# Kernel optimization log

Measured on AMD Instinct MI355X. Metric: run time of the kernel, lower is better.

The kernel has to match this reference:

```python
import jax, jax.numpy as jnp
import numpy as np

EPS = 1e-08  # smooth in CELoss


def _lovasz_grad(fg_sorted):
    # Alg. 1 of the Lovasz-Softmax paper; fg_sorted: [P] floats in {0,1}
    gts = fg_sorted.sum()
    intersection = gts - jnp.cumsum(fg_sorted)
    union = gts + jnp.cumsum(1.0 - fg_sorted)
    jaccard = 1.0 - intersection / union
    # first-difference: jaccard[1:] - jaccard[:-1], keep jaccard[0]
    return jnp.concatenate([jaccard[:1], jaccard[1:] - jaccard[:-1]])


def setup_inputs() -> dict:
    key = jax.random.key(0)
    k1, k2 = jax.random.split(key)
    B, C, D, H, W = 1, 3, 96, 256, 256
    probas = jax.random.normal(k1, (B, C, D, H, W), dtype=jnp.float32)
    cls = jax.random.randint(k2, (B, D, H, W), 0, C)
    # one-hot label volume [B, C, D, H, W], matching labels[0][c] == 1 usage
    labels = jax.nn.one_hot(cls, C, axis=1, dtype=jnp.int32)
    weight = jnp.ones((C,), dtype=jnp.float32)  # weight=[1,1,1]
    return {"probas": probas, "weight": weight, "labels": labels}


def reference(probas, weight, labels):
    C = probas.shape[1]
    # flatten_probas (dim==5 path): softmax over classes, flatten to [P, C]
    p = jax.nn.softmax(probas, axis=1)
    p = jnp.moveaxis(p, 1, -1).reshape(-1, C)
    # label reconstruction: 0*ch0 + 1*ch1 + 2*ch2 from one-hot channels
    lab = (labels[0, 1] + 2 * labels[0, 2]).reshape(-1)  # [P] int class ids

    total = jnp.zeros((), dtype=p.dtype)
    count = jnp.zeros((), dtype=p.dtype)
    for c in range(C):
        fg = (lab == c).astype(p.dtype)              # [P]
        present = fg.sum() > 0                       # classes='present'
        # CELoss(softmax=False, average='None'): -fg * log(pred + eps)
        errors = -fg * jnp.log(p[:, c] + EPS)        # [P]
        order = jnp.argsort(-errors)                 # descending sort perm
        errors_sorted = errors[order]
        fg_sorted = fg[order]
        g = jax.lax.stop_gradient(_lovasz_grad(fg_sorted))
        loss_c = weight[c] * jnp.dot(errors_sorted, g)
        total = total + jnp.where(present, loss_c, 0.0)
        count = count + jnp.where(present, 1.0, 0.0)
    # mean over present classes (empty -> 0)
    return jnp.where(count > 0, total / jnp.maximum(count, 1.0), 0.0)
```

## Files before the change

kernel.cpp:

```cpp
#include <hip/hip_runtime.h>


#define EPS 1e-8f
#define BLK 256
#define GPT 6
#define GPB (GPT*BLK)

typedef float fx4 __attribute__((ext_vector_type(4)));
typedef int   ix4 __attribute__((ext_vector_type(4)));

__device__ __forceinline__ void px_acc(float za, float zb, float zc, int la, int lb,
                                       float& s0, float& s1, float& s2,
                                       float& n0, float& n1, float& n2)
{
    float ea = __expf(za);
    float eb = __expf(zb);
    float ec = __expf(zc);
    float d  = ea + eb + ec;
    float zl = (la != 0) ? zb : ((lb != 0) ? zc : za);
    float err = __logf(d) - zl;
    float f1 = (la != 0) ? 1.f : 0.f;
    float f2 = (lb != 0) ? 1.f : 0.f;
    float f0 = 1.f - f1 - f2;
    s0 += f0 * err;  s1 += f1 * err;  s2 += f2 * err;
    n0 += f0;        n1 += f1;        n2 += f2;
}

__global__ __launch_bounds__(BLK) void lovasz_reduce_kernel(
    const float* __restrict__ probas,
    const int*   __restrict__ labels,
    float* __restrict__ partial,
    int P4, int P, int nfull, int nblocks)
{
    const fx4* z0 = (const fx4*)(probas);
    const fx4* z1 = (const fx4*)(probas + (size_t)P);
    const fx4* z2 = (const fx4*)(probas + 2 * (size_t)P);
    const ix4* l1 = (const ix4*)(labels + (size_t)P);
    const ix4* l2 = (const ix4*)(labels + 2 * (size_t)P);

    float s0 = 0.f, s1 = 0.f, s2 = 0.f;
    float n0 = 0.f, n1 = 0.f, n2 = 0.f;

    const int base = blockIdx.x * GPB + threadIdx.x;

    if (blockIdx.x < nfull) {
        #pragma unroll
        for (int j = 0; j < GPT; ++j) {
            int i = base + j * BLK;
            fx4 a = z0[i];
            fx4 b = z1[i];
            fx4 c = z2[i];
            ix4 u = l1[i];
            ix4 v = l2[i];
            px_acc(a.x, b.x, c.x, u.x, v.x, s0, s1, s2, n0, n1, n2);
            px_acc(a.y, b.y, c.y, u.y, v.y, s0, s1, s2, n0, n1, n2);
            px_acc(a.z, b.z, c.z, u.z, v.z, s0, s1, s2, n0, n1, n2);
            px_acc(a.w, b.w, c.w, u.w, v.w, s0, s1, s2, n0, n1, n2);
        }
    } else {
        #pragma unroll
        for (int j = 0; j < GPT; ++j) {
            int i = base + j * BLK;
            if (i < P4) {
                fx4 a = z0[i];
                fx4 b = z1[i];
                fx4 c = z2[i];
                ix4 u = l1[i];
                ix4 v = l2[i];
                px_acc(a.x, b.x, c.x, u.x, v.x, s0, s1, s2, n0, n1, n2);
                px_acc(a.y, b.y, c.y, u.y, v.y, s0, s1, s2, n0, n1, n2);
                px_acc(a.z, b.z, c.z, u.z, v.z, s0, s1, s2, n0, n1, n2);
                px_acc(a.w, b.w, c.w, u.w, v.w, s0, s1, s2, n0, n1, n2);
            }
        }
    }

    #pragma unroll
    for (int off = 32; off > 0; off >>= 1) {
        s0 += __shfl_down(s0, off);
        s1 += __shfl_down(s1, off);
        s2 += __shfl_down(s2, off);
        n0 += __shfl_down(n0, off);
        n1 += __shfl_down(n1, off);
        n2 += __shfl_down(n2, off);
    }

    __shared__ float red[6][4];
    int wave = threadIdx.x >> 6;
    int lane = threadIdx.x & 63;
    if (lane == 0) {
        red[0][wave] = s0; red[1][wave] = s1; red[2][wave] = s2;
        red[3][wave] = n0; red[4][wave] = n1; red[5][wave] = n2;
    }
    __syncthreads();
    if (threadIdx.x < 6) {
        int k = threadIdx.x;
        partial[(size_t)k * nblocks + blockIdx.x] =
            red[k][0] + red[k][1] + red[k][2] + red[k][3];
    }
}

__global__ __launch_bounds__(256) void lovasz_finalize_kernel(
    const float* __restrict__ partial, int nblocks,
    const float* __restrict__ probas, const int* __restrict__ labels,
    const float* __restrict__ weight, float* __restrict__ out,
    int P4, int P)
{
    float acc[6] = {0.f, 0.f, 0.f, 0.f, 0.f, 0.f};
    for (int b = threadIdx.x; b < nblocks; b += 256) {
        #pragma unroll
        for (int k = 0; k < 6; ++k)
            acc[k] += partial[(size_t)k * nblocks + b];
    }

    #pragma unroll
    for (int k = 0; k < 6; ++k)
        #pragma unroll
        for (int off = 32; off > 0; off >>= 1)
            acc[k] += __shfl_down(acc[k], off);

    __shared__ float red[6][4];
    int wave = threadIdx.x >> 6;
    int lane = threadIdx.x & 63;
    if (lane == 0) {
        #pragma unroll
        for (int k = 0; k < 6; ++k) red[k][wave] = acc[k];
    }
    __syncthreads();
    if (threadIdx.x == 0) {
        float s[6];
        #pragma unroll
        for (int k = 0; k < 6; ++k)
            s[k] = red[k][0] + red[k][1] + red[k][2] + red[k][3];
        for (int i = 4 * P4; i < P; ++i) {
            px_acc(probas[i], probas[(size_t)P + i], probas[2 * (size_t)P + i],
                   labels[(size_t)P + i], labels[2 * (size_t)P + i],
                   s[0], s[1], s[2], s[3], s[4], s[5]);
        }
        float total = 0.f, cnt = 0.f;
        #pragma unroll
        for (int c = 0; c < 3; ++c) {
            if (s[3 + c] > 0.f) {
                total += weight[c] * s[c] / s[3 + c];
                cnt += 1.f;
            }
        }
        out[0] = (cnt > 0.f) ? total / cnt : 0.f;
    }
}

extern "C" void kernel_launch(void* const* d_in, const int* in_sizes, int n_in,
                              void* d_out, int out_size, void* d_ws, size_t ws_size,
                              hipStream_t stream) {
    const float* probas = (const float*)d_in[0];
    const float* weight = (const float*)d_in[1];
    const int*   labels = (const int*)d_in[2];
    float* partial = (float*)d_ws;

    int total = in_sizes[0];
    int P  = total / 3;
    int P4 = P / 4;
    int nfull = P4 / GPB;
    int rem = P4 - nfull * GPB;
    int nblocks = nfull + (rem ? 1 : 0);

    lovasz_reduce_kernel<<<nblocks, BLK, 0, stream>>>(probas, labels, partial,
                                                      P4, P, nfull, nblocks);
    lovasz_finalize_kernel<<<1, 256, 0, stream>>>(partial, nblocks, probas,
                                                  labels, weight, (float*)d_out,
                                                  P4, P);
}
```

Before: 167.2 us.

## Stage per-stream loads through LDS with one wave per input stream

```diff
diff --git a/kernel.cpp b/kernel.cpp
--- a/kernel.cpp
+++ b/kernel.cpp
@@ -2,12 +2,15 @@
 
 
 #define EPS 1e-8f
-#define BLK 256
-#define GPT 6
-#define GPB (GPT*BLK)
+#define BLK 320
+#define CHK 320
+#define CHUNKS 6
+#define GPB (CHK*CHUNKS)
 
 typedef float fx4 __attribute__((ext_vector_type(4)));
 typedef int   ix4 __attribute__((ext_vector_type(4)));
+
+#define NTL(p) __builtin_nontemporal_load(p)
 
 __device__ __forceinline__ void px_acc(float za, float zb, float zc, int la, int lb,
                                        float& s0, float& s1, float& s2,
@@ -32,46 +35,70 @@
     float* __restrict__ partial,
     int P4, int P, int nfull, int nblocks)
 {
-    const fx4* z0 = (const fx4*)(probas);
-    const fx4* z1 = (const fx4*)(probas + (size_t)P);
-    const fx4* z2 = (const fx4*)(probas + 2 * (size_t)P);
-    const ix4* l1 = (const ix4*)(labels + (size_t)P);
-    const ix4* l2 = (const ix4*)(labels + 2 * (size_t)P);
+    const fx4* z0  = (const fx4*)(probas);
+    const fx4* z1  = (const fx4*)(probas + (size_t)P);
+    const fx4* z2  = (const fx4*)(probas + 2 * (size_t)P);
+    const fx4* l1f = (const fx4*)(labels + (size_t)P);
+    const fx4* l2f = (const fx4*)(labels + 2 * (size_t)P);
+    const ix4* l1  = (const ix4*)(labels + (size_t)P);
+    const ix4* l2  = (const ix4*)(labels + 2 * (size_t)P);
+
+    __shared__ fx4 lds[5][CHK];
 
     float s0 = 0.f, s1 = 0.f, s2 = 0.f;
     float n0 = 0.f, n1 = 0.f, n2 = 0.f;
 
-    const int base = blockIdx.x * GPB + threadIdx.x;
+    const int t    = threadIdx.x;
+    const int wave = t >> 6;
+    const int lane = t & 63;
 
     if (blockIdx.x < nfull) {
-        #pragma unroll
-        for (int j = 0; j < GPT; ++j) {
-            int i = base + j * BLK;
-            fx4 a = z0[i];
-            fx4 b = z1[i];
-            fx4 c = z2[i];
-            ix4 u = l1[i];
-            ix4 v = l2[i];
-            px_acc(a.x, b.x, c.x, u.x, v.x, s0, s1, s2, n0, n1, n2);
-            px_acc(a.y, b.y, c.y, u.y, v.y, s0, s1, s2, n0, n1, n2);
-            px_acc(a.z, b.z, c.z, u.z, v.z, s0, s1, s2, n0, n1, n2);
-            px_acc(a.w, b.w, c.w, u.w, v.w, s0, s1, s2, n0, n1, n2);
-        }
-    } else {
-        #pragma unroll
-        for (int j = 0; j < GPT; ++j) {
-            int i = base + j * BLK;
-            if (i < P4) {
-                fx4 a = z0[i];
-                fx4 b = z1[i];
-                fx4 c = z2[i];
-                ix4 u = l1[i];
-                ix4 v = l2[i];
+        const int bb = blockIdx.x * GPB;
+        const fx4* src;
+        if      (wave == 0) src = z0;
+        else if (wave == 1) src = z1;
+        else if (wave == 2) src = z2;
+        else if (wave == 3) src = l1f;
+        else                src = l2f;
+
+        #pragma unroll 1
+        for (int ch = 0; ch < CHUNKS; ++ch) {
+            const int cb = bb + ch * CHK;
+            fx4 r0 = NTL(&src[cb + 0 * 64 + lane]);
+            fx4 r1 = NTL(&src[cb + 1 * 64 + lane]);
+            fx4 r2 = NTL(&src[cb + 2 * 64 + lane]);
+            fx4 r3 = NTL(&src[cb + 3 * 64 + lane]);
+            fx4 r4 = NTL(&src[cb + 4 * 64 + lane]);
+            lds[wave][0 * 64 + lane] = r0;
+            lds[wave][1 * 64 + lane] = r1;
+            lds[wave][2 * 64 + lane] = r2;
+            lds[wave][3 * 64 + lane] = r3;
+            lds[wave][4 * 64 + lane] = r4;
+            __syncthreads();
+            {
+                fx4 a = lds[0][t];
+                fx4 b = lds[1][t];
+                fx4 c = lds[2][t];
+                ix4 u = *(ix4*)&lds[3][t];
+                ix4 v = *(ix4*)&lds[4][t];
                 px_acc(a.x, b.x, c.x, u.x, v.x, s0, s1, s2, n0, n1, n2);
                 px_acc(a.y, b.y, c.y, u.y, v.y, s0, s1, s2, n0, n1, n2);
                 px_acc(a.z, b.z, c.z, u.z, v.z, s0, s1, s2, n0, n1, n2);
                 px_acc(a.w, b.w, c.w, u.w, v.w, s0, s1, s2, n0, n1, n2);
             }
+            __syncthreads();
+        }
+    } else {
+        for (int i = blockIdx.x * GPB + t; i < P4; i += BLK) {
+            fx4 a = NTL(&z0[i]);
+            fx4 b = NTL(&z1[i]);
+            fx4 c = NTL(&z2[i]);
+            ix4 u = NTL(&l1[i]);
+            ix4 v = NTL(&l2[i]);
+            px_acc(a.x, b.x, c.x, u.x, v.x, s0, s1, s2, n0, n1, n2);
+            px_acc(a.y, b.y, c.y, u.y, v.y, s0, s1, s2, n0, n1, n2);
+            px_acc(a.z, b.z, c.z, u.z, v.z, s0, s1, s2, n0, n1, n2);
+            px_acc(a.w, b.w, c.w, u.w, v.w, s0, s1, s2, n0, n1, n2);
         }
     }
 
@@ -85,18 +112,16 @@
         n2 += __shfl_down(n2, off);
     }
 
-    __shared__ float red[6][4];
-    int wave = threadIdx.x >> 6;
-    int lane = threadIdx.x & 63;
+    __shared__ float red[6][5];
     if (lane == 0) {
         red[0][wave] = s0; red[1][wave] = s1; red[2][wave] = s2;
         red[3][wave] = n0; red[4][wave] = n1; red[5][wave] = n2;
     }
     __syncthreads();
-    if (threadIdx.x < 6) {
-        int k = threadIdx.x;
+    if (t < 6) {
+        int k = t;
         partial[(size_t)k * nblocks + blockIdx.x] =
-            red[k][0] + red[k][1] + red[k][2] + red[k][3];
+            red[k][0] + red[k][1] + red[k][2] + red[k][3] + red[k][4];
     }
 }
 
```

New measurement: 158.1 us. 5.4% less time.
